# Optimization experiments

Hardware: AMD Instinct MI355X
Metric: run time of the kernel (lower is better)

Reference implementation:

```python
import math
import jax, jax.numpy as jnp
import numpy as np

B = 512
E = 512
C = 70722
M_MARGIN = 0.4
H = 0.333
S = 64.0
T_ALPHA = 1.0
EPS = 1e-3


def setup_inputs() -> dict:
    key = jax.random.key(0)
    k1, k2, k3, k4 = jax.random.split(key, 4)
    embbedings = jax.random.normal(k1, (B, E), dtype=jnp.float32)
    embbedings = embbedings / jnp.linalg.norm(embbedings, axis=1, keepdims=True)
    # feature norms typically ~[10, 30] for face models
    norms = 10.0 + 20.0 * jax.random.uniform(k2, (B, 1), dtype=jnp.float32)
    label = jax.random.randint(k3, (B,), 0, C, dtype=jnp.int64)
    kernel = jax.random.normal(k4, (E, C), dtype=jnp.float32)
    batch_mean = jnp.ones((C,), dtype=jnp.float32) * 20.0
    batch_std = jnp.asarray(10.0, dtype=jnp.float32)
    return {"embbedings": embbedings, "norms": norms, "label": label,
            "kernel": kernel, "batch_mean": batch_mean, "batch_std": batch_std}


def reference(embbedings, norms, label, kernel, batch_mean, batch_std):
    # column-wise l2-normalize the class weight matrix [E, C]
    kernel_norm = kernel / jnp.linalg.norm(kernel, axis=0, keepdims=True)
    cosine = jnp.clip(embbedings @ kernel_norm, -1.0 + EPS, 1.0 - EPS)  # [B, C]
    safe_norms = jnp.clip(norms, 1e-3, 100.0)  # [B, 1]

    # ---- running-stat update (torch.no_grad block) ----
    sn = jax.lax.stop_gradient(safe_norms[:, 0])  # [B]
    sums = jnp.zeros((C,), dtype=sn.dtype).at[label].add(sn)
    counts = jnp.zeros((C,), dtype=sn.dtype).at[label].add(1.0)
    group_mean = sums / jnp.maximum(counts, 1.0)  # per-class batch mean of norms
    new_mean = jnp.where(counts > 0,
                         group_mean * T_ALPHA + (1.0 - T_ALPHA) * batch_mean,
                         batch_mean)
    std = jnp.std(sn, ddof=1)  # torch.std is unbiased
    new_std = std * T_ALPHA + (1.0 - T_ALPHA) * batch_std

    # ---- adaptive margin ----
    margin_scaler = (safe_norms - new_mean[label][:, None]) / (new_std + EPS)
    margin_scaler = jnp.clip(margin_scaler * H, -1.0, 1.0)  # [B, 1]

    oh = jax.nn.one_hot(label, C, dtype=cosine.dtype)  # [B, C]
    g_angular = -M_MARGIN * margin_scaler               # [B, 1]
    theta = jnp.arccos(cosine)
    theta_m = jnp.clip(theta + oh * g_angular, EPS, math.pi - EPS)
    g_add = M_MARGIN + M_MARGIN * margin_scaler         # [B, 1]
    out = (jnp.cos(theta_m) - oh * g_add) * S
    return out
```

## Files before the change

### kernel.cpp

```cpp
#include <hip/hip_runtime.h>
#include <hip/hip_bf16.h>
#include <cstdint>
#include <cstddef>
#include <math.h>

#define B_SZ 512
#define E_SZ 512
#define C_SZ 70722
#define PAD_C 70784
#define M_MARGIN 0.4f
#define H_CONST 0.333f
#define S_CONST 64.0f
#define EPS_F 1e-3f
#define PI_F 3.14159265358979323846f

typedef __attribute__((ext_vector_type(8))) short short8;
typedef __attribute__((ext_vector_type(4))) float f32x4;


__device__ __forceinline__ unsigned short f2bf(float x) {
  __hip_bfloat16 h = __float2bfloat16(x);
  unsigned short u;
  __builtin_memcpy(&u, &h, 2);
  return u;
}

__device__ __forceinline__ void gload_lds16(const void* g, void* l) {
  __builtin_amdgcn_global_load_lds(
      (const __attribute__((address_space(1))) unsigned int*)g,
      (__attribute__((address_space(3))) unsigned int*)l, 16, 0, 0);
}

__device__ __forceinline__ int swzb(int rc) {
  return (((rc & 7) ^ ((rc >> 2) & 7)) << 4);
}

__global__ void k_stats(const float* __restrict__ norms, const int* __restrict__ label,
                        float* __restrict__ ga, float* __restrict__ gadd) {
  __shared__ float sn[B_SZ];
  __shared__ int lab[B_SZ];
  __shared__ float redA[8], redB[8];
  __shared__ float sh_std;

  int t = threadIdx.x;
  float v = norms[t];
  v = fminf(fmaxf(v, 1e-3f), 100.0f);
  sn[t] = v;
  lab[t] = label[t];

  float s1 = v, s2 = v * v;
  #pragma unroll
  for (int o = 32; o > 0; o >>= 1) {
    s1 += __shfl_down(s1, o);
    s2 += __shfl_down(s2, o);
  }
  if ((t & 63) == 0) { redA[t >> 6] = s1; redB[t >> 6] = s2; }
  __syncthreads();
  if (t == 0) {
    float a = 0.f, b = 0.f;
    #pragma unroll
    for (int i = 0; i < 8; ++i) { a += redA[i]; b += redB[i]; }
    float mean = a / (float)B_SZ;
    float var = (b - (float)B_SZ * mean * mean) / (float)(B_SZ - 1);
    sh_std = sqrtf(fmaxf(var, 0.f));
  }
  __syncthreads();
  float stdv = sh_std;

  int myl = lab[t];
  float s = 0.f, cnt = 0.f;
  for (int j = 0; j < B_SZ; ++j) {
    bool m = (lab[j] == myl);
    s += m ? sn[j] : 0.f;
    cnt += m ? 1.f : 0.f;
  }
  float gm = s / fmaxf(cnt, 1.f);
  float ms = (v - gm) / (stdv + EPS_F) * H_CONST;
  ms = fminf(fmaxf(ms, -1.f), 1.f);
  ga[t] = -M_MARGIN * ms;
  gadd[t] = M_MARGIN + M_MARGIN * ms;
}

__global__ void k_cvtA(const float* __restrict__ emb, unsigned short* __restrict__ abf) {
  int i = (blockIdx.x * 256 + threadIdx.x) * 4;
  float4 f = *(const float4*)(emb + i);
  unsigned short u0 = f2bf(f.x), u1 = f2bf(f.y), u2 = f2bf(f.z), u3 = f2bf(f.w);
  unsigned long long pk = (unsigned long long)u0 | ((unsigned long long)u1 << 16) |
                          ((unsigned long long)u2 << 32) | ((unsigned long long)u3 << 48);
  *(unsigned long long*)(abf + i) = pk;
}

__global__ void k_prep(const float* __restrict__ K, float* __restrict__ invn,
                       unsigned short* __restrict__ BT) {
  __shared__ float T[64 * 64];
  __shared__ float part[16][64];

  const int t = threadIdx.x;
  const int c0 = blockIdx.x * 64;
  const int cl = t & 15;
  const int kr = t >> 4;
  const int cq = t >> 2;
  const int kq = t & 3;
  const bool full = (c0 + 64 <= C_SZ);

  float ss0 = 0.f, ss1 = 0.f, ss2 = 0.f, ss3 = 0.f;

  for (int ch = 0; ch < 8; ++ch) {
    if (ch) __syncthreads();
    #pragma unroll
    for (int i = 0; i < 4; ++i) {
      int klo = kr + i * 16;
      int kg = ch * 64 + klo;
      float4 f;
      if (full) {
        f = *(const float4*)(K + (size_t)kg * C_SZ + c0 + cl * 4);
      } else {
        float* fp = (float*)&f;
        #pragma unroll
        for (int j = 0; j < 4; ++j) {
          int c = c0 + cl * 4 + j;
          fp[j] = (c < C_SZ) ? K[(size_t)kg * C_SZ + c] : 0.f;
        }
      }
      ss0 += f.x * f.x; ss1 += f.y * f.y; ss2 += f.z * f.z; ss3 += f.w * f.w;
      int swz = (klo & 7) << 2;
      *(float4*)&T[klo * 64 + ((cl * 4) ^ swz)] = f;
    }
    __syncthreads();
    #pragma unroll
    for (int sub = 0; sub < 2; ++sub) {
      int k8 = sub * 32 + kq * 8;
      short8 v;
      #pragma unroll
      for (int i = 0; i < 8; ++i) {
        v[i] = (short)f2bf(T[(k8 + i) * 64 + (cq ^ (i << 2))]);
      }
      *(short8*)(BT + ((size_t)(c0 + cq) << 9) + ch * 64 + k8) = v;
    }
  }

  __syncthreads();
  part[kr][cl * 4 + 0] = ss0;
  part[kr][cl * 4 + 1] = ss1;
  part[kr][cl * 4 + 2] = ss2;
  part[kr][cl * 4 + 3] = ss3;
  __syncthreads();
  if (t < 64) {
    int c = c0 + t;
    float s = 0.f;
    #pragma unroll
    for (int r = 0; r < 16; ++r) s += part[r][t];
    invn[c] = (c < C_SZ) ? rsqrtf(s) : 0.f;
  }
}

__launch_bounds__(256)
__global__ void k_gemm_fast(const unsigned short* __restrict__ Abf,
                            const unsigned short* __restrict__ BT,
                            const float* __restrict__ invn,
                            const int* __restrict__ label,
                            const float* __restrict__ ga,
                            const float* __restrict__ gadd,
                            float* __restrict__ out) {
  __shared__ __align__(16) unsigned short As[128 * 64];
  __shared__ __align__(16) unsigned short Bs[128 * 64];
  __shared__ int lab_s[128];
  __shared__ float ga_s[128], gadd_s[128];

  const int tid = threadIdx.x;
  const int nwg = gridDim.x;
  int bid = blockIdx.x;

  int q = nwg >> 3, r8 = nwg & 7;
  int xcd = bid & 7, lb = bid >> 3;
  int wg = (xcd < r8 ? xcd * (q + 1) : r8 * (q + 1) + (xcd - r8) * q) + lb;

  const int mt = wg & 3;
  const int nt = wg >> 2;
  const int row0 = mt << 7;
  const int col0 = nt << 7;

  if (tid < 128) {
    int gr = row0 + tid;
    lab_s[tid] = label[gr];
    ga_s[tid] = ga[gr];
    gadd_s[tid] = gadd[gr];
  }

  const int wid = tid >> 6, lane = tid & 63;
  const int wr = wid >> 1, wc = wid & 1;

  f32x4 acc[4][4];
  #pragma unroll
  for (int m = 0; m < 4; ++m)
    #pragma unroll
    for (int n = 0; n < 4; ++n)
      acc[m][n] = f32x4{0.f, 0.f, 0.f, 0.f};

  const int rsub = lane >> 3;
  const int lchunk = lane & 7;

  for (int kt = 0; kt < 8; ++kt) {
    const int kb = kt * 64;
    if (kt) __syncthreads();

    #pragma unroll
    for (int rr = 0; rr < 4; ++rr) {
      int rowblk = wid * 32 + rr * 8;
      int r = rowblk + rsub;
      int s = lchunk ^ ((r & 7) ^ ((r >> 2) & 7));
      gload_lds16(Abf + (size_t)(row0 + r) * 512 + kb + s * 8,
                  (char*)As + rowblk * 128);
      gload_lds16(BT + (size_t)(col0 + r) * 512 + kb + s * 8,
                  (char*)Bs + rowblk * 128);
    }

    __syncthreads();

    #pragma unroll
    for (int ks = 0; ks < 2; ++ks) {
      short8 a[4], b[4];
      #pragma unroll
      for (int m = 0; m < 4; ++m) {
        int row = wr * 64 + m * 16 + (lane & 15);
        int off = (row * 128 + ks * 64 + (lane >> 4) * 16) ^ swzb(row);
        a[m] = *(const short8*)((const char*)As + off);
      }
      #pragma unroll
      for (int n = 0; n < 4; ++n) {
        int c = wc * 64 + n * 16 + (lane & 15);
        int off = (c * 128 + ks * 64 + (lane >> 4) * 16) ^ swzb(c);
        b[n] = *(const short8*)((const char*)Bs + off);
      }
      #pragma unroll
      for (int m = 0; m < 4; ++m)
        #pragma unroll
        for (int n = 0; n < 4; ++n)
          acc[m][n] = __builtin_amdgcn_mfma_f32_16x16x32_bf16(a[m], b[n], acc[m][n], 0, 0, 0);
    }
  }

  float invc[4];
  #pragma unroll
  for (int n = 0; n < 4; ++n)
    invc[n] = invn[col0 + wc * 64 + n * 16 + (lane & 15)];

  #pragma unroll
  for (int m = 0; m < 4; ++m) {
    int rl0 = wr * 64 + m * 16 + ((lane >> 4) << 2);
    #pragma unroll
    for (int n = 0; n < 4; ++n) {
      int cl = wc * 64 + n * 16 + (lane & 15);
      int gc = col0 + cl;
      if (gc >= C_SZ) continue;
      #pragma unroll
      for (int r = 0; r < 4; ++r) {
        int rl = rl0 + r;
        float v = acc[m][n][r] * invc[n];
        v = fminf(fmaxf(v, -1.f + EPS_F), 1.f - EPS_F);
        float res = v * S_CONST;
        if (gc == lab_s[rl]) {
          float th = acosf(v) + ga_s[rl];
          th = fminf(fmaxf(th, EPS_F), PI_F - EPS_F);
          res = (cosf(th) - gadd_s[rl]) * S_CONST;
        }
        out[(size_t)(row0 + rl) * C_SZ + gc] = res;
      }
    }
  }
}


__global__ void k_colnorm(const float* __restrict__ K, float* __restrict__ inv) {
  __shared__ float part[4][64];
  int cl = threadIdx.x & 63;
  int rq = threadIdx.x >> 6;
  int c = blockIdx.x * 64 + cl;
  float s = 0.f;
  if (c < C_SZ) {
    const float* p = K + (size_t)rq * 128 * C_SZ + c;
    #pragma unroll 8
    for (int r = 0; r < 128; ++r) {
      float x = p[(size_t)r * C_SZ];
      s += x * x;
    }
  }
  part[rq][cl] = s;
  __syncthreads();
  if (threadIdx.x < 64) {
    int c2 = blockIdx.x * 64 + threadIdx.x;
    if (c2 < C_SZ) {
      float tt = part[0][threadIdx.x] + part[1][threadIdx.x] +
                 part[2][threadIdx.x] + part[3][threadIdx.x];
      inv[c2] = rsqrtf(tt);
    } else if (c2 < PAD_C) {
      inv[c2] = 0.f;
    }
  }
}

__launch_bounds__(256)
__global__ void k_gemm_fb(const unsigned short* __restrict__ Abf,
                          const float* __restrict__ Kmat,
                          const float* __restrict__ invn,
                          const int* __restrict__ label,
                          const float* __restrict__ ga,
                          const float* __restrict__ gadd,
                          float* __restrict__ out) {
  __shared__ __align__(16) unsigned short As[128 * 64];
  __shared__ __align__(16) unsigned short Bs[128 * 64];
  __shared__ int lab_s[128];
  __shared__ float ga_s[128], gadd_s[128];

  const int tid = threadIdx.x;
  const int nwg = gridDim.x;
  int bid = blockIdx.x;
  int q = nwg >> 3, r8 = nwg & 7;
  int xcd = bid & 7, lb = bid >> 3;
  int wg = (xcd < r8 ? xcd * (q + 1) : r8 * (q + 1) + (xcd - r8) * q) + lb;
  const int mt = wg & 3;
  const int nt = wg >> 2;
  const int row0 = mt << 7;
  const int col0 = nt << 7;

  if (tid < 128) {
    int gr = row0 + tid;
    lab_s[tid] = label[gr];
    ga_s[tid] = ga[gr];
    gadd_s[tid] = gadd[gr];
  }

  const int wid = tid >> 6, lane = tid & 63;
  const int wr = wid >> 1, wc = wid & 1;
  const int cc = tid & 31;
  const int kq = tid >> 5;
  const bool edge = (col0 + 128 > C_SZ);
  float4 inv4 = *(const float4*)(invn + col0 + cc * 4);

  f32x4 acc[4][4];
  #pragma unroll
  for (int m = 0; m < 4; ++m)
    #pragma unroll
    for (int n = 0; n < 4; ++n)
      acc[m][n] = f32x4{0.f, 0.f, 0.f, 0.f};

  const float* Bg = Kmat + col0;

  for (int kt = 0; kt < 8; ++kt) {
    const int kb = kt * 64;
    if (kt) __syncthreads();

    #pragma unroll
    for (int rr = 0; rr < 4; ++rr) {
      int rowblk = wid * 32 + rr * 8;
      int r = rowblk + (lane >> 3);
      int s = (lane & 7) ^ ((r & 7) ^ ((r >> 2) & 7));
      gload_lds16(Abf + (size_t)(row0 + r) * 512 + kb + s * 8, (char*)As + rowblk * 128);
    }

    #pragma unroll
    for (int i = 0; i < 4; ++i) {
      int k = (kq + i * 8) * 2;
      const float* g0 = Bg + (size_t)(kb + k) * C_SZ + cc * 4;
      const float* g1 = g0 + C_SZ;
      float x0[4], x1[4];
      if (!edge) {
        float4 f0 = *(const float4*)g0;
        float4 f1 = *(const float4*)g1;
        x0[0]=f0.x; x0[1]=f0.y; x0[2]=f0.z; x0[3]=f0.w;
        x1[0]=f1.x; x1[1]=f1.y; x1[2]=f1.z; x1[3]=f1.w;
      } else {
        #pragma unroll
        for (int j = 0; j < 4; ++j) {
          int gc = col0 + cc * 4 + j;
          x0[j] = (gc < C_SZ) ? g0[j] : 0.f;
          x1[j] = (gc < C_SZ) ? g1[j] : 0.f;
        }
      }
      #pragma unroll
      for (int j = 0; j < 4; ++j) {
        int c = cc * 4 + j;
        float iv = ((const float*)&inv4)[j];
        unsigned int pk = ((unsigned int)f2bf(x1[j] * iv) << 16) | (unsigned int)f2bf(x0[j] * iv);
        int byte = (c * 128 + k * 2) ^ swzb(c);
        *(unsigned int*)((char*)Bs + byte) = pk;
      }
    }

    __syncthreads();

    #pragma unroll
    for (int ks = 0; ks < 2; ++ks) {
      short8 a[4], b[4];
      #pragma unroll
      for (int m = 0; m < 4; ++m) {
        int row = wr * 64 + m * 16 + (lane & 15);
        int off = (row * 128 + ks * 64 + (lane >> 4) * 16) ^ swzb(row);
        a[m] = *(const short8*)((const char*)As + off);
      }
      #pragma unroll
      for (int n = 0; n < 4; ++n) {
        int c = wc * 64 + n * 16 + (lane & 15);
        int off = (c * 128 + ks * 64 + (lane >> 4) * 16) ^ swzb(c);
        b[n] = *(const short8*)((const char*)Bs + off);
      }
      #pragma unroll
      for (int m = 0; m < 4; ++m)
        #pragma unroll
        for (int n = 0; n < 4; ++n)
          acc[m][n] = __builtin_amdgcn_mfma_f32_16x16x32_bf16(a[m], b[n], acc[m][n], 0, 0, 0);
    }
  }

  #pragma unroll
  for (int m = 0; m < 4; ++m) {
    int rl0 = wr * 64 + m * 16 + ((lane >> 4) << 2);
    #pragma unroll
    for (int n = 0; n < 4; ++n) {
      int cl = wc * 64 + n * 16 + (lane & 15);
      int gc = col0 + cl;
      if (gc >= C_SZ) continue;
      #pragma unroll
      for (int r = 0; r < 4; ++r) {
        int rl = rl0 + r;
        float v = acc[m][n][r];
        v = fminf(fmaxf(v, -1.f + EPS_F), 1.f - EPS_F);
        float res = v * S_CONST;
        if (gc == lab_s[rl]) {
          float th = acosf(v) + ga_s[rl];
          th = fminf(fmaxf(th, EPS_F), PI_F - EPS_F);
          res = (cosf(th) - gadd_s[rl]) * S_CONST;
        }
        out[(size_t)(row0 + rl) * C_SZ + gc] = res;
      }
    }
  }
}

extern "C" void kernel_launch(void* const* d_in, const int* in_sizes, int n_in,
                              void* d_out, int out_size, void* d_ws, size_t ws_size,
                              hipStream_t stream) {
  const float* emb   = (const float*)d_in[0];
  const float* norms = (const float*)d_in[1];
  const int*   label = (const int*)d_in[2];
  const float* kmat  = (const float*)d_in[3];
  float* out = (float*)d_out;

  const size_t NEED_FAST = 73294336;
  char* ws = (char*)d_ws;
  float* invn = (float*)ws;
  float* ga   = (float*)(ws + 283136);
  float* gadd = (float*)(ws + 285184);
  unsigned short* abf = (unsigned short*)(ws + 287232);
  unsigned short* bt  = (unsigned short*)(ws + 811520);

  k_stats<<<1, 512, 0, stream>>>(norms, label, ga, gadd);
  k_cvtA<<<256, 256, 0, stream>>>(emb, abf);

  if (ws_size >= NEED_FAST) {
    k_prep<<<1106, 256, 0, stream>>>(kmat, invn, bt);
    k_gemm_fast<<<2212, 256, 0, stream>>>(abf, bt, invn, label, ga, gadd, out);
  } else {
    k_colnorm<<<1106, 256, 0, stream>>>(kmat, invn);
    k_gemm_fb<<<2212, 256, 0, stream>>>(abf, kmat, invn, label, ga, gadd, out);
  }
}
```

Before: 150.1 us.

## Double-buffer B tile in LDS and stream A fragments directly into registers

The GEMM main loop now double-buffers only the B (class-weight) tile in LDS. The A (embedding) fragments are loaded straight from global memory into registers one k-step ahead, instead of being staged through LDS. This cuts the loop to one barrier per step and lets the next B tile's global-to-LDS copy overlap with the current MFMA work. It also raises wave priority around the MFMA blocks and precomputes the swizzled B offsets. The cost is more VGPRs for the prefetched A fragments and less coalesced direct global reads of A, which rely on cache hits.

```diff
diff --git a/kernel.cpp b/kernel.cpp
--- a/kernel.cpp
+++ b/kernel.cpp
@@ -162,8 +162,7 @@
                             const float* __restrict__ ga,
                             const float* __restrict__ gadd,
                             float* __restrict__ out) {
-  __shared__ __align__(16) unsigned short As[128 * 64];
-  __shared__ __align__(16) unsigned short Bs[128 * 64];
+  __shared__ __align__(16) unsigned short Bs[2][128 * 64];
   __shared__ int lab_s[128];
   __shared__ float ga_s[128], gadd_s[128];
 
@@ -171,9 +170,9 @@
   const int nwg = gridDim.x;
   int bid = blockIdx.x;
 
-  int q = nwg >> 3, r8 = nwg & 7;
+  int q8 = nwg >> 3, r8 = nwg & 7;
   int xcd = bid & 7, lb = bid >> 3;
-  int wg = (xcd < r8 ? xcd * (q + 1) : r8 * (q + 1) + (xcd - r8) * q) + lb;
+  int wg = (xcd < r8 ? xcd * (q8 + 1) : r8 * (q8 + 1) + (xcd - r8) * q8) + lb;
 
   const int mt = wg & 3;
   const int nt = wg >> 2;
@@ -189,6 +188,21 @@
 
   const int wid = tid >> 6, lane = tid & 63;
   const int wr = wid >> 1, wc = wid & 1;
+  const int q = lane >> 4;
+  const int l15 = lane & 15;
+
+  const char* const aB0 =
+      (const char*)(Abf + (size_t)(row0 + wr * 64 + l15) * 512 + q * 8);
+
+  const int rsub = lane >> 3;
+  const int lchunk = lane & 7;
+
+  int offB[4];
+  #pragma unroll
+  for (int n = 0; n < 4; ++n) {
+    int c = wc * 64 + n * 16 + l15;
+    offB[n] = (c * 128 + q * 16) ^ swzb(c);
+  }
 
   f32x4 acc[4][4];
   #pragma unroll
@@ -197,60 +211,70 @@
     for (int n = 0; n < 4; ++n)
       acc[m][n] = f32x4{0.f, 0.f, 0.f, 0.f};
 
-  const int rsub = lane >> 3;
-  const int lchunk = lane & 7;
-
-  for (int kt = 0; kt < 8; ++kt) {
-    const int kb = kt * 64;
-    if (kt) __syncthreads();
-
-    #pragma unroll
-    for (int rr = 0; rr < 4; ++rr) {
-      int rowblk = wid * 32 + rr * 8;
-      int r = rowblk + rsub;
-      int s = lchunk ^ ((r & 7) ^ ((r >> 2) & 7));
-      gload_lds16(Abf + (size_t)(row0 + r) * 512 + kb + s * 8,
-                  (char*)As + rowblk * 128);
-      gload_lds16(BT + (size_t)(col0 + r) * 512 + kb + s * 8,
-                  (char*)Bs + rowblk * 128);
-    }
-
-    __syncthreads();
-
-    #pragma unroll
-    for (int ks = 0; ks < 2; ++ks) {
-      short8 a[4], b[4];
-      #pragma unroll
-      for (int m = 0; m < 4; ++m) {
-        int row = wr * 64 + m * 16 + (lane & 15);
-        int off = (row * 128 + ks * 64 + (lane >> 4) * 16) ^ swzb(row);
-        a[m] = *(const short8*)((const char*)As + off);
-      }
-      #pragma unroll
-      for (int n = 0; n < 4; ++n) {
-        int c = wc * 64 + n * 16 + (lane & 15);
-        int off = (c * 128 + ks * 64 + (lane >> 4) * 16) ^ swzb(c);
-        b[n] = *(const short8*)((const char*)Bs + off);
-      }
-      #pragma unroll
-      for (int m = 0; m < 4; ++m)
-        #pragma unroll
-        for (int n = 0; n < 4; ++n)
-          acc[m][n] = __builtin_amdgcn_mfma_f32_16x16x32_bf16(a[m], b[n], acc[m][n], 0, 0, 0);
-    }
-  }
+  short8 a[4][2];
+
+#define BSTAGE(BUF, KT)                                                      \
+  { _Pragma("unroll")                                                        \
+    for (int rr_ = 0; rr_ < 4; ++rr_) {                                      \
+      int rowblk_ = wid * 32 + rr_ * 8;                                      \
+      int r_ = rowblk_ + rsub;                                               \
+      int s_ = lchunk ^ ((r_ & 7) ^ ((r_ >> 2) & 7));                        \
+      gload_lds16(BT + (size_t)(col0 + r_) * 512 + (KT) * 64 + s_ * 8,       \
+                  (char*)&Bs[BUF][0] + rowblk_ * 128);                       \
+    } }
+
+#define AISSUE(KT)                                                           \
+  { _Pragma("unroll")                                                        \
+    for (int m_ = 0; m_ < 4; ++m_) {                                         \
+      a[m_][0] = *(const short8*)(aB0 + m_ * 16384 + (KT) * 128);            \
+      a[m_][1] = *(const short8*)(aB0 + m_ * 16384 + (KT) * 128 + 64);       \
+    } }
+
+#define COMPUTE(BUF)                                                         \
+  { _Pragma("unroll")                                                        \
+    for (int ks_ = 0; ks_ < 2; ++ks_) {                                      \
+      short8 b_[4];                                                          \
+      _Pragma("unroll")                                                      \
+      for (int n_ = 0; n_ < 4; ++n_)                                         \
+        b_[n_] = *(const short8*)((const char*)&Bs[BUF][0] +                 \
+                                  (offB[n_] ^ (ks_ * 64)));                  \
+      __builtin_amdgcn_s_setprio(1);                                         \
+      _Pragma("unroll")                                                      \
+      for (int m_ = 0; m_ < 4; ++m_)                                         \
+        _Pragma("unroll")                                                    \
+        for (int n_ = 0; n_ < 4; ++n_)                                       \
+          acc[m_][n_] = __builtin_amdgcn_mfma_f32_16x16x32_bf16(             \
+              a[m_][ks_], b_[n_], acc[m_][n_], 0, 0, 0);                     \
+      __builtin_amdgcn_s_setprio(0);                                         \
+    } }
+
+#define STEP(KT)                                                             \
+  __syncthreads();                         \
+  { if ((KT) < 7) BSTAGE(((KT) + 1) & 1, (KT) + 1) }                         \
+  COMPUTE((KT) & 1)                                                          \
+  { if ((KT) < 7) AISSUE((KT) + 1) }
+
+  BSTAGE(0, 0)
+  AISSUE(0)
+
+  STEP(0) STEP(1) STEP(2) STEP(3) STEP(4) STEP(5) STEP(6) STEP(7)
+
+#undef STEP
+#undef COMPUTE
+#undef AISSUE
+#undef BSTAGE
 
   float invc[4];
   #pragma unroll
   for (int n = 0; n < 4; ++n)
-    invc[n] = invn[col0 + wc * 64 + n * 16 + (lane & 15)];
+    invc[n] = invn[col0 + wc * 64 + n * 16 + l15];
 
   #pragma unroll
   for (int m = 0; m < 4; ++m) {
-    int rl0 = wr * 64 + m * 16 + ((lane >> 4) << 2);
+    int rl0 = wr * 64 + m * 16 + (q << 2);
     #pragma unroll
     for (int n = 0; n < 4; ++n) {
-      int cl = wc * 64 + n * 16 + (lane & 15);
+      int cl = wc * 64 + n * 16 + l15;
       int gc = col0 + cl;
       if (gc >= C_SZ) continue;
       #pragma unroll
```

After: 181.8 us. 21.1% more time.
